# Kernel tuning notes

Measured on AMD Instinct MI355X. Metric: run time of the kernel, lower is better.

## Reference

```python
import jax, jax.numpy as jnp
import numpy as np

N = 50000          # number of nodes
A = 32             # anchor_set_num
D = 64             # latdim


def setup_inputs() -> dict:
    key = jax.random.key(0)
    k1, k2, k3, k4, k5 = jax.random.split(key, 5)
    embeds = jax.random.normal(k1, (N, D), dtype=jnp.float32)
    dists_array = jax.random.uniform(k2, (A, N), dtype=jnp.float32)
    anchor_set_id = jax.random.randint(k3, (A,), 0, N)
    # nn.Linear(2*latdim, latdim): weight [D, 2D], bias [D]
    bound = 1.0 / np.sqrt(2 * D)
    W_hidden = jax.random.uniform(k4, (D, 2 * D), minval=-bound, maxval=bound, dtype=jnp.float32)
    b_hidden = jax.random.uniform(k5, (D,), minval=-bound, maxval=bound, dtype=jnp.float32)
    return {"embeds": embeds, "dists_array": dists_array,
            "anchor_set_id": anchor_set_id,
            "W_hidden": W_hidden, "b_hidden": b_hidden}


def reference(embeds, dists_array, anchor_set_id, W_hidden, b_hidden):
    n, d = embeds.shape
    a = anchor_set_id.shape[0]
    # set_ids_emb.repeat(N,1).reshape(N, A, D) reduces to broadcasting anchors over nodes
    set_ids_emb = embeds[anchor_set_id]                       # [A, D]
    # messages[n, a] = set_ids_emb[a] * dists[a, n]
    messages = set_ids_emb[None, :, :] * dists_array.T[:, :, None]   # [N, A, D]
    # embeds.repeat(A,1).reshape(N, A, D): element [i, j] = embeds[(i*A + j) % N]
    self_feature = jnp.tile(embeds, (a, 1)).reshape(n, a, d)         # [N, A, D]
    # concat + Linear(2D -> D) expressed as split matmul (same math, no concat buffer)
    W1 = W_hidden[:, :d]   # acts on messages
    W2 = W_hidden[:, d:]   # acts on self_feature
    hidden = (jnp.einsum('nad,kd->nak', messages, W1)
              + jnp.einsum('nad,kd->nak', self_feature, W2)
              + b_hidden)                                            # [N, A, D]
    return jnp.mean(hidden, axis=1)                                  # [N, D]
```

## Files before the change

### kernel.cpp

```cpp
#include <hip/hip_runtime.h>


typedef float f32x4 __attribute__((ext_vector_type(4)));

constexpr int N_PTS  = 50000;
constexpr int A_ANCH = 32;
constexpr int D_DIM  = 64;
constexpr int NSB    = 3125;
constexpr int TN     = 16;
constexpr int TILES  = N_PTS / TN;
constexpr int XSTR   = 36;
constexpr int PREP_TILE   = 8;
constexpr int PREP_BLOCKS = (NSB + PREP_TILE - 1) / PREP_TILE;
constexpr int MAIN_GRID   = 782;

__global__ __launch_bounds__(256) void prep_kernel(
        const float* __restrict__ embeds,
        const int*   __restrict__ aid,
        const float* __restrict__ W,
        float*       __restrict__ M1,
        float*       __restrict__ SBW)
{
    const int t = threadIdx.x;

    if (blockIdx.x == PREP_BLOCKS) {
        for (int idx = t; idx < A_ANCH * D_DIM; idx += 256) {
            int a = idx >> 6, k = idx & 63;
            const float* erow = embeds + (size_t)aid[a] * D_DIM;
            const float* wrow = W + (size_t)k * 128;
            float s = 0.0f;
#pragma unroll
            for (int d = 0; d < D_DIM; ++d) s += erow[d] * wrow[d];
            M1[idx] = s * (1.0f / 32.0f);
        }
        return;
    }

    __shared__ float w2[64 * 64];
    __shared__ float sb[PREP_TILE * 64];

    {
        int k  = t & 63;
        int d0 = (t >> 6) * 16;
        const float* wr = W + (size_t)k * 128 + 64;
#pragma unroll
        for (int q = 0; q < 16; ++q) w2[(d0 + q) * 64 + k] = wr[d0 + q];
    }

    const int i0 = blockIdx.x * PREP_TILE;
    {
        int d = t & 63, il = t >> 6;
        for (; il < PREP_TILE; il += 4) {
            int i = i0 + il;
            if (i >= NSB) break;
            int base = 16 * i;
            float s = 0.0f;
#pragma unroll
            for (int j = 0; j < 32; ++j) {
                int r = base + j;
                if (r >= N_PTS) r -= N_PTS;
                s += embeds[(size_t)r * D_DIM + d];
            }
            sb[il * 64 + d] = s;
        }
    }
    __syncthreads();
    {
        int k = t & 63, il = t >> 6;
        for (; il < PREP_TILE; il += 4) {
            int i = i0 + il;
            if (i >= NSB) break;
            const float* srow = sb + il * 64;
            float s = 0.0f;
#pragma unroll
            for (int d = 0; d < D_DIM; ++d) s += srow[d] * w2[d * 64 + k];
            SBW[(size_t)i * 64 + k] = s * (1.0f / 32.0f);
        }
    }
}

__global__ __launch_bounds__(256, 4) void pnn_main(
        const float* __restrict__ dists,
        const float* __restrict__ b,
        const float* __restrict__ M1,
        const float* __restrict__ SBW,
        float*       __restrict__ out)
{
    __shared__ float m1s[A_ANCH * D_DIM];
    __shared__ float xs[2][TN * XSTR];

    const int t = threadIdx.x;

    {
        const float4* M4 = (const float4*)M1;
        float4*       s4 = (float4*)m1s;
#pragma unroll
        for (int q = 0; q < 2; ++q) s4[t + 256 * q] = M4[t + 256 * q];
    }

    const int lane_k  = t & 15;
    const int n_local = t >> 4;
    const int k0      = lane_k * 4;
    const float4 bias = *(const float4*)(b + k0);

    const int st_a  = t >> 4;
    const int st_nl = t & 15;

    {
        const int n0 = blockIdx.x * TN;
#pragma unroll
        for (int q = 0; q < 2; ++q) {
            int a = st_a + 16 * q;
            xs[0][st_nl * XSTR + a] =
                __builtin_nontemporal_load(dists + (size_t)a * N_PTS + n0 + st_nl);
        }
    }
    __syncthreads();

    int tile = blockIdx.x;
    for (int g = 0; tile < TILES; ++g, tile += MAIN_GRID) {
        const int cur = g & 1;
        const int n   = tile * TN + n_local;
        const int i   = (2 * n) % NSB;
        float4 sbw = *(const float4*)(SBW + (size_t)i * D_DIM + k0);

        const int ntile = tile + MAIN_GRID;
        if (ntile < TILES) {
            const int n0 = ntile * TN;
#pragma unroll
            for (int q = 0; q < 2; ++q) {
                int a = st_a + 16 * q;
                xs[cur ^ 1][st_nl * XSTR + a] =
                    __builtin_nontemporal_load(dists + (size_t)a * N_PTS + n0 + st_nl);
            }
        }

        float4 acc;
        acc.x = bias.x + sbw.x; acc.y = bias.y + sbw.y;
        acc.z = bias.z + sbw.z; acc.w = bias.w + sbw.w;

        const float* xrow = xs[cur] + n_local * XSTR;
#pragma unroll
        for (int jj = 0; jj < A_ANCH; jj += 4) {
            float4 xv = *(const float4*)(xrow + jj);
            float4 w0 = *(const float4*)(m1s + (jj + 0) * 64 + k0);
            float4 w1 = *(const float4*)(m1s + (jj + 1) * 64 + k0);
            float4 w2 = *(const float4*)(m1s + (jj + 2) * 64 + k0);
            float4 w3 = *(const float4*)(m1s + (jj + 3) * 64 + k0);
            acc.x += xv.x * w0.x; acc.y += xv.x * w0.y; acc.z += xv.x * w0.z; acc.w += xv.x * w0.w;
            acc.x += xv.y * w1.x; acc.y += xv.y * w1.y; acc.z += xv.y * w1.z; acc.w += xv.y * w1.w;
            acc.x += xv.z * w2.x; acc.y += xv.z * w2.y; acc.z += xv.z * w2.z; acc.w += xv.z * w2.w;
            acc.x += xv.w * w3.x; acc.y += xv.w * w3.y; acc.z += xv.w * w3.z; acc.w += xv.w * w3.w;
        }
        {
            f32x4 accv;
            accv.x = acc.x; accv.y = acc.y; accv.z = acc.z; accv.w = acc.w;
            __builtin_nontemporal_store(accv, (f32x4*)(out + (size_t)n * D_DIM + k0));
        }

        __syncthreads();
    }
}

extern "C" void kernel_launch(void* const* d_in, const int* in_sizes, int n_in,
                              void* d_out, int out_size, void* d_ws, size_t ws_size,
                              hipStream_t stream) {
    const float* embeds = (const float*)d_in[0];
    const float* dists  = (const float*)d_in[1];
    const int*   aid    = (const int*)  d_in[2];
    const float* W      = (const float*)d_in[3];
    const float* b      = (const float*)d_in[4];
    float*       out    = (float*)d_out;

    float* M1  = (float*)d_ws;
    float* SBW = (float*)d_ws + A_ANCH * D_DIM;

    prep_kernel<<<PREP_BLOCKS + 1, 256, 0, stream>>>(embeds, aid, W, M1, SBW);
    pnn_main<<<MAIN_GRID, 256, 0, stream>>>(dists, b, M1, SBW, out);
}
```

Baseline: 102.4 us.

## Replace persistent double-buffered loop with one 128-node tile per block

The main kernel no longer loops persistently over 16-node tiles with double-buffered shared memory and a barrier per tile. Each block now handles one 128-node tile: it stages all 32x128 dists values at once and computes 8 output rows per thread, so each weight float4 read from shared memory is reused across 8 nodes. This removes the per-tile barriers and improves register-level reuse of the weights. In exchange it launches about 391 non-persistent blocks, uses more registers, loses load/compute overlap within a block, and adds clamping for the partial last tile.

```diff
diff --git a/kernel.cpp b/kernel.cpp
--- a/kernel.cpp
+++ b/kernel.cpp
@@ -7,12 +7,11 @@
 constexpr int A_ANCH = 32;
 constexpr int D_DIM  = 64;
 constexpr int NSB    = 3125;
-constexpr int TN     = 16;
-constexpr int TILES  = N_PTS / TN;
+constexpr int TN     = 128;
+constexpr int MAIN_GRID = (N_PTS + TN - 1) / TN;
 constexpr int XSTR   = 36;
 constexpr int PREP_TILE   = 8;
 constexpr int PREP_BLOCKS = (NSB + PREP_TILE - 1) / PREP_TILE;
-constexpr int MAIN_GRID   = 782;
 
 __global__ __launch_bounds__(256) void prep_kernel(
         const float* __restrict__ embeds,
@@ -87,9 +86,10 @@
         float*       __restrict__ out)
 {
     __shared__ float m1s[A_ANCH * D_DIM];
-    __shared__ float xs[2][TN * XSTR];
+    __shared__ float xs[TN * XSTR];
 
-    const int t = threadIdx.x;
+    const int t  = threadIdx.x;
+    const int n0 = blockIdx.x * TN;
 
     {
         const float4* M4 = (const float4*)M1;
@@ -97,68 +97,58 @@
 #pragma unroll
         for (int q = 0; q < 2; ++q) s4[t + 256 * q] = M4[t + 256 * q];
     }
-
-    const int lane_k  = t & 15;
-    const int n_local = t >> 4;
-    const int k0      = lane_k * 4;
-    const float4 bias = *(const float4*)(b + k0);
-
-    const int st_a  = t >> 4;
-    const int st_nl = t & 15;
-
     {
-        const int n0 = blockIdx.x * TN;
 #pragma unroll
-        for (int q = 0; q < 2; ++q) {
-            int a = st_a + 16 * q;
-            xs[0][st_nl * XSTR + a] =
-                __builtin_nontemporal_load(dists + (size_t)a * N_PTS + n0 + st_nl);
+        for (int q = 0; q < 16; ++q) {
+            int idx = t + 256 * q;
+            int a   = idx >> 7;
+            int nl  = idx & 127;
+            int col = n0 + nl; if (col >= N_PTS) col = N_PTS - 1;
+            xs[nl * XSTR + a] =
+                __builtin_nontemporal_load(dists + (size_t)a * N_PTS + col);
         }
     }
     __syncthreads();
 
-    int tile = blockIdx.x;
-    for (int g = 0; tile < TILES; ++g, tile += MAIN_GRID) {
-        const int cur = g & 1;
-        const int n   = tile * TN + n_local;
-        const int i   = (2 * n) % NSB;
+    const int lane_k  = t & 15;
+    const int nl_base = t >> 4;
+    const int k0      = lane_k * 4;
+    const float4 bias = *(const float4*)(b + k0);
+
+    float4 acc[8];
+#pragma unroll
+    for (int q = 0; q < 8; ++q) {
+        int n = n0 + nl_base + 16 * q;
+        int nc = (n < N_PTS) ? n : (N_PTS - 1);
+        int i  = (2 * nc) % NSB;
         float4 sbw = *(const float4*)(SBW + (size_t)i * D_DIM + k0);
+        acc[q].x = bias.x + sbw.x; acc[q].y = bias.y + sbw.y;
+        acc[q].z = bias.z + sbw.z; acc[q].w = bias.w + sbw.w;
+    }
 
-        const int ntile = tile + MAIN_GRID;
-        if (ntile < TILES) {
-            const int n0 = ntile * TN;
 #pragma unroll
-            for (int q = 0; q < 2; ++q) {
-                int a = st_a + 16 * q;
-                xs[cur ^ 1][st_nl * XSTR + a] =
-                    __builtin_nontemporal_load(dists + (size_t)a * N_PTS + n0 + st_nl);
-            }
+    for (int jj = 0; jj < A_ANCH; jj += 4) {
+        float4 w0 = *(const float4*)(m1s + (jj + 0) * 64 + k0);
+        float4 w1 = *(const float4*)(m1s + (jj + 1) * 64 + k0);
+        float4 w2 = *(const float4*)(m1s + (jj + 2) * 64 + k0);
+        float4 w3 = *(const float4*)(m1s + (jj + 3) * 64 + k0);
+#pragma unroll
+        for (int q = 0; q < 8; ++q) {
+            float4 xv = *(const float4*)(xs + (nl_base + 16 * q) * XSTR + jj);
+            acc[q].x += xv.x * w0.x; acc[q].y += xv.x * w0.y; acc[q].z += xv.x * w0.z; acc[q].w += xv.x * w0.w;
+            acc[q].x += xv.y * w1.x; acc[q].y += xv.y * w1.y; acc[q].z += xv.y * w1.z; acc[q].w += xv.y * w1.w;
+            acc[q].x += xv.z * w2.x; acc[q].y += xv.z * w2.y; acc[q].z += xv.z * w2.z; acc[q].w += xv.z * w2.w;
+            acc[q].x += xv.w * w3.x; acc[q].y += xv.w * w3.y; acc[q].z += xv.w * w3.z; acc[q].w += xv.w * w3.w;
         }
+    }
 
-        float4 acc;
-        acc.x = bias.x + sbw.x; acc.y = bias.y + sbw.y;
-        acc.z = bias.z + sbw.z; acc.w = bias.w + sbw.w;
-
-        const float* xrow = xs[cur] + n_local * XSTR;
 #pragma unroll
-        for (int jj = 0; jj < A_ANCH; jj += 4) {
-            float4 xv = *(const float4*)(xrow + jj);
-            float4 w0 = *(const float4*)(m1s + (jj + 0) * 64 + k0);
-            float4 w1 = *(const float4*)(m1s + (jj + 1) * 64 + k0);
-            float4 w2 = *(const float4*)(m1s + (jj + 2) * 64 + k0);
-            float4 w3 = *(const float4*)(m1s + (jj + 3) * 64 + k0);
-            acc.x += xv.x * w0.x; acc.y += xv.x * w0.y; acc.z += xv.x * w0.z; acc.w += xv.x * w0.w;
-            acc.x += xv.y * w1.x; acc.y += xv.y * w1.y; acc.z += xv.y * w1.z; acc.w += xv.y * w1.w;
-            acc.x += xv.z * w2.x; acc.y += xv.z * w2.y; acc.z += xv.z * w2.z; acc.w += xv.z * w2.w;
-            acc.x += xv.w * w3.x; acc.y += xv.w * w3.y; acc.z += xv.w * w3.z; acc.w += xv.w * w3.w;
+    for (int q = 0; q < 8; ++q) {
+        int n = n0 + nl_base + 16 * q;
+        if (n < N_PTS) {
+            f32x4 av; av.x = acc[q].x; av.y = acc[q].y; av.z = acc[q].z; av.w = acc[q].w;
+            __builtin_nontemporal_store(av, (f32x4*)(out + (size_t)n * D_DIM + k0));
         }
-        {
-            f32x4 accv;
-            accv.x = acc.x; accv.y = acc.y; accv.z = acc.z; accv.w = acc.w;
-            __builtin_nontemporal_store(accv, (f32x4*)(out + (size_t)n * D_DIM + k0));
-        }
-
-        __syncthreads();
     }
 }
 
```

New measurement: 160.4 us. 1.57x slower.
